# Kernel tuning notes

Hardware: AMD Instinct MI355X
Metric: run time of the kernel (lower is better)

Reference implementation:

```python
import jax, jax.numpy as jnp
import numpy as np

ALPHA, BETA, THETA = 1.0, 1.0, 10.0
WIN_SIZE = 11
SIGMA = 1.5


def _gauss_window(size, sigma, channel):
    g = np.exp(-((np.arange(size) - size // 2) ** 2) / (2.0 * sigma ** 2))
    g = g / g.sum()
    w2 = np.outer(g, g).astype(np.float32)  # [k, k]
    return jnp.asarray(np.tile(w2[None, None], (channel, 1, 1, 1)))  # [C,1,k,k]


def _dwconv_valid(x, w):
    # x: [B,C,H,W], w: [C,1,k,k]; depthwise conv, no padding (matches F.conv2d padd=0, groups=C)
    return jax.lax.conv_general_dilated(
        x, w, window_strides=(1, 1), padding='VALID',
        feature_group_count=x.shape[1],
        dimension_numbers=('NCHW', 'OIHW', 'NCHW'))


def _ssim_loss(img1, img2, window):
    # val_range heuristic: inputs in [0,1) -> L = 1
    L = 1.0
    C1 = (0.01 * L) ** 2
    C2 = (0.03 * L) ** 2
    mu1 = _dwconv_valid(img1, window)
    mu2 = _dwconv_valid(img2, window)
    mu1_sq = mu1 * mu1
    mu2_sq = mu2 * mu2
    mu1_mu2 = mu1 * mu2
    sigma1_sq = _dwconv_valid(img1 * img1, window) - mu1_sq
    sigma2_sq = _dwconv_valid(img2 * img2, window) - mu2_sq
    sigma12 = _dwconv_valid(img1 * img2, window) - mu1_mu2
    v1 = 2.0 * sigma12 + C2
    v2 = sigma1_sq + sigma2_sq + C2
    ssim_map = (2.0 * mu1_mu2 + C1) * v1 / ((mu1_sq + mu2_sq + C1) * v2)
    return 1.0 - jnp.mean(ssim_map)


_LAP2D = np.array([[1.0, 1.0, 1.0],
                   [1.0, -8.0, 1.0],
                   [1.0, 1.0, 1.0]], dtype=np.float32) / 16.0  # kornia normalized (abs-sum=16)


def _laplacian(x):
    # kornia.filters.laplacian(x, 3): reflect padding, normalized 3x3 laplacian, depthwise
    c = x.shape[1]
    k = jnp.asarray(np.tile(_LAP2D[None, None], (c, 1, 1, 1)))  # [C,1,3,3]
    xp = jnp.pad(x, ((0, 0), (0, 0), (1, 1), (1, 1)), mode='reflect')
    return _dwconv_valid(xp, k)


def setup_inputs() -> dict:
    key = jax.random.key(0)
    ks = jax.random.split(key, 5)
    shape = (32, 1, 512, 512)
    names = ['im_fus', 'im_ir', 'im_vi', 'map_ir', 'map_vi']
    return {n: jax.random.uniform(k, shape, dtype=jnp.float32) for n, k in zip(names, ks)}


def reference(im_fus, im_ir, im_vi, map_ir, map_vi):
    window = _gauss_window(WIN_SIZE, SIGMA, im_fus.shape[1])
    ms_ssim_loss = _ssim_loss(im_fus, im_ir, window) + _ssim_loss(im_fus, im_vi, window)
    l1_loss = jnp.mean(jnp.abs(jnp.maximum(map_ir, map_vi) - im_fus))
    ir_grad = jnp.abs(_laplacian(im_ir))
    vi_grad = jnp.abs(_laplacian(im_vi))
    fus_grad = jnp.abs(_laplacian(im_fus))
    grad_loss = jnp.mean(jnp.abs(jnp.maximum(ir_grad, vi_grad) - fus_grad))
    return ALPHA * ms_ssim_loss + BETA * l1_loss + THETA * grad_loss
```

## Files before the change

### kernel.cpp

```cpp
#include <hip/hip_runtime.h>
#include <cmath>


typedef float f32x2 __attribute__((ext_vector_type(2)));

struct GaussW { float w[11]; };

#define SSIM_C1 1.0e-4f
#define SSIM_C2 9.0e-4f

__global__ __launch_bounds__(256, 2)
void ssim_kernel(const float* __restrict__ fus, const float* __restrict__ irp,
                 const float* __restrict__ vip, const float* __restrict__ mir,
                 const float* __restrict__ mvi, float* __restrict__ ws,
                 GaussW gw)
{
    const int b    = blockIdx.z;
    const int rs   = blockIdx.y;
    const int r0   = rs * 42;
    const int tid  = threadIdx.x;
    const int wv   = tid >> 6;
    const int lane = tid & 63;
    const int c0   = blockIdx.x * 256 + wv * 64;
    const int out_rows = min(42, 502 - r0);
    const int in_rows  = out_rows + 10;
    const bool first = (rs == 0);
    const bool last  = (rs == 11);

    const size_t ib = (size_t)b * 512 * 512;
    const float* __restrict__ Fp = fus + ib;
    const float* __restrict__ Ip = irp + ib;
    const float* __restrict__ Vp = vip + ib;
    mir += ib;
    mvi += ib;

    __shared__ f32x2 srow_fi[4][80];
    __shared__ float srow_v [4][80];

    float w6[6];
#pragma unroll
    for (int k = 0; k < 6; ++k) w6[k] = gw.w[k];

    f32x2 acc[11][4];
#pragma unroll
    for (int s = 0; s < 11; ++s)
#pragma unroll
        for (int q = 0; q < 4; ++q) acc[s][q] = (f32x2)(0.f);

    float lssim = 0.f, l1s = 0.f, grs = 0.f;
    const int  col      = c0 + lane;
    const bool col_ok   = col <= 501;
    const bool is_left  = (lane == 10);
    const int  colH     = is_left ? (c0 - 1) : (c0 + 64 + lane);
    const bool halo_ok  = (lane < 10) ? (colH < 512) : (is_left && c0 > 0);
    const int  hidx     = 64 + lane;
    const int il       = (lane == 0) ? ((c0 == 0) ? 1 : 74) : (lane - 1);
    const bool rt_edge = (lane == 63) && (c0 + 64 >= 512);

    f32x2 csFI_1 = (f32x2)(0.f), csFI_2 = (f32x2)(0.f);
    float csV_1 = 0.f, csV_2 = 0.f;
    f32x2 cPrevFI = (f32x2)(0.f); float cPrevV = 0.f;
    float m1r = 0.f, m2r = 0.f;

    float rf, rg, rv, rf2 = 0.f, rg2 = 0.f, rv2 = 0.f;
    {
        const size_t b0 = (size_t)r0 * 512 + col;
        rf = Fp[b0]; rg = Ip[b0]; rv = Vp[b0];
        if (halo_ok) {
            const size_t bh = (size_t)r0 * 512 + colH;
            rf2 = Fp[bh]; rg2 = Ip[bh]; rv2 = Vp[bh];
        }
    }

#pragma unroll 1
    for (int rb = 0; rb < 55; rb += 11) {
#pragma unroll
        for (int p = 0; p < 11; ++p) {
            const int r = rb + p;
            if (r < in_rows) {
                const float curF = rf, curI = rg, curV = rv;
                srow_fi[wv][lane] = (f32x2){rf, rg};
                srow_v [wv][lane] = rv;
                if (halo_ok) {
                    srow_fi[wv][hidx] = (f32x2){rf2, rg2};
                    srow_v [wv][hidx] = rv2;
                }
                __builtin_amdgcn_wave_barrier();

                if (r + 1 < in_rows) {
                    const size_t base = (size_t)(r0 + r + 1) * 512 + col;
                    rf = Fp[base]; rg = Ip[base]; rv = Vp[base];
                    if (halo_ok) {
                        const size_t bh = (size_t)(r0 + r + 1) * 512 + colH;
                        rf2 = Fp[bh]; rg2 = Ip[bh]; rv2 = Vp[bh];
                    }
                }

                f32x2 hfhi  = (f32x2)(0.f);
                f32x2 hffii = (f32x2)(0.f);
                f32x2 hfifv = (f32x2)(0.f);
                f32x2 hvvv  = (f32x2)(0.f);
                f32x2 fi1 = (f32x2)(0.f); float v1 = 0.f;
#pragma unroll
                for (int k = 0; k < 11; ++k) {
                    const float t = w6[k < 6 ? k : 10 - k];
                    const f32x2 fi = srow_fi[wv][lane + k];
                    const float V  = srow_v [wv][lane + k];
                    if (k == 1) { fi1 = fi; v1 = V; }
                    const f32x2 t2 = (f32x2){t, t};
                    const f32x2 tfi = t2 * fi;
                    hfhi  = __builtin_elementwise_fma(t2,  fi, hfhi);
                    hffii = __builtin_elementwise_fma(tfi, fi, hffii);
                    hfifv.x = fmaf(tfi.x, fi.y, hfifv.x);
                    hfifv.y = fmaf(tfi.x, V,    hfifv.y);
                    const float tV = t * V;
                    hvvv.x = fmaf(t,  V, hvvv.x);
                    hvvv.y = fmaf(tV, V, hvvv.y);
                }

                const bool lap_row = (r <= 43) || last;
                f32x2 csFI_cur = (f32x2)(0.f); float csV_cur = 0.f;
                if (lap_row) {
                    const f32x2 fiL = srow_fi[wv][il];
                    const float vL  = srow_v [wv][il];
                    f32x2 fiR = fi1; float vR = v1;
                    if (rt_edge) { fiR = fiL; vR = vL; }
                    csFI_cur = fiL + fiR + (f32x2){curF, curI};
                    csV_cur  = vL  + vR  + curV;
                }
                __builtin_amdgcn_wave_barrier();

                {
                    const f32x2 w02 = (f32x2){w6[0], w6[0]};
                    acc[p][0] = w02 * hfhi;
                    acc[p][1] = w02 * hffii;
                    acc[p][2] = w02 * hfifv;
                    acc[p][3] = w02 * hvvv;
                }
#pragma unroll
                for (int k = 1; k < 11; ++k) {
                    const int s = (p - k + 11) % 11;
                    const float t = w6[k < 6 ? k : 10 - k];
                    const f32x2 t2 = (f32x2){t, t};
                    acc[s][0] = __builtin_elementwise_fma(t2, hfhi,  acc[s][0]);
                    acc[s][1] = __builtin_elementwise_fma(t2, hffii, acc[s][1]);
                    acc[s][2] = __builtin_elementwise_fma(t2, hfifv, acc[s][2]);
                    acc[s][3] = __builtin_elementwise_fma(t2, hvvv,  acc[s][3]);
                }
                if (r >= 10) {
                    const int s = (p + 1) % 11;
                    const float mu1 = acc[s][0].x, mu2 = acc[s][0].y, mu3 = acc[s][3].x;
                    const float eff = acc[s][1].x, eii = acc[s][1].y, evv = acc[s][3].y;
                    const float efi = acc[s][2].x, efv = acc[s][2].y;
                    const float mu1sq = mu1*mu1, mu2sq = mu2*mu2, mu3sq = mu3*mu3;
                    const float mu12 = mu1*mu2, mu13 = mu1*mu3;
                    const float sf  = eff - mu1sq;
                    const float si  = eii - mu2sq;
                    const float sv  = evv - mu3sq;
                    const float s12 = efi - mu12;
                    const float s13 = efv - mu13;
                    const float n1 = (2.f*mu12 + SSIM_C1) * (2.f*s12 + SSIM_C2);
                    const float d1 = (mu1sq + mu2sq + SSIM_C1) * (sf + si + SSIM_C2);
                    const float n2 = (2.f*mu13 + SSIM_C1) * (2.f*s13 + SSIM_C2);
                    const float d2 = (mu1sq + mu3sq + SSIM_C1) * (sf + sv + SSIM_C2);
                    const float q1 = __builtin_amdgcn_rcpf(d1);
                    const float q2 = __builtin_amdgcn_rcpf(d2);
                    if (col_ok) lssim += fmaf(n1, q1, n2 * q2);
                }
                if (r >= 2 && lap_row) {
                    const f32x2 sFI = csFI_2 + csFI_1 + csFI_cur;
                    const float sV  = csV_2 + csV_1 + csV_cur;
                    const f32x2 lFI = __builtin_elementwise_fma(
                                         (f32x2){-9.f,-9.f}, cPrevFI, sFI);
                    const float lV  = fmaf(-9.f, cPrevV, sV);
                    grs += fabsf(fmaxf(fabsf(lFI.y), fabsf(lV)) - fabsf(lFI.x));
                    l1s += fabsf(fmaxf(m1r, m2r) - cPrevFI.x);
                }
                if (first && r == 1) {
                    const f32x2 sFI = csFI_1 + csFI_cur + csFI_cur;
                    const float sV  = csV_1 + csV_cur + csV_cur;
                    const f32x2 lFI = __builtin_elementwise_fma(
                                         (f32x2){-9.f,-9.f}, cPrevFI, sFI);
                    const float lV  = fmaf(-9.f, cPrevV, sV);
                    grs += fabsf(fmaxf(fabsf(lFI.y), fabsf(lV)) - fabsf(lFI.x));
                    l1s += fabsf(fmaxf(m1r, m2r) - cPrevFI.x);
                }
                if (lap_row) {
                    csFI_2 = csFI_1; csFI_1 = csFI_cur;
                    csV_2  = csV_1;  csV_1  = csV_cur;
                    cPrevFI = (f32x2){curF, curI}; cPrevV = curV;
                    const int ny = min(r0 + r, 511);
                    const size_t bm = (size_t)ny * 512 + col;
                    m1r = mir[bm]; m2r = mvi[bm];
                }
            }
        }
    }

    if (last) {
        const size_t bm = (size_t)511 * 512 + col;
        const float m1e = mir[bm], m2e = mvi[bm];
        const f32x2 sFI = csFI_2 + csFI_2 + csFI_1;
        const float sV  = csV_2 + csV_2 + csV_1;
        const f32x2 lFI = __builtin_elementwise_fma((f32x2){-9.f,-9.f}, cPrevFI, sFI);
        const float lV  = fmaf(-9.f, cPrevV, sV);
        grs += fabsf(fmaxf(fabsf(lFI.y), fabsf(lV)) - fabsf(lFI.x));
        l1s += fabsf(fmaxf(m1e, m2e) - cPrevFI.x);
    }

#pragma unroll
    for (int off = 32; off > 0; off >>= 1) {
        lssim += __shfl_down(lssim, off);
        l1s   += __shfl_down(l1s, off);
        grs   += __shfl_down(grs, off);
    }
    __shared__ float red[12];
    if (lane == 0) { red[wv] = lssim; red[4 + wv] = l1s; red[8 + wv] = grs; }
    __syncthreads();
    if (tid == 0) {
        const int blk = blockIdx.x + 2 * (blockIdx.y + 12 * blockIdx.z);
        ws[blk]        = red[0] + red[1] + red[2] + red[3];
        ws[768 + blk]  = red[4] + red[5] + red[6] + red[7];
        ws[1536 + blk] = (red[8] + red[9] + red[10] + red[11]) * 0.0625f;
    }
}

__global__ void final_kernel(const float* __restrict__ ws, float* __restrict__ out)
{
    const int tid = threadIdx.x;
    float s0 = 0.f, s1 = 0.f, s2 = 0.f;
#pragma unroll
    for (int i = tid; i < 768; i += 256) {
        s0 += ws[i];
        s1 += ws[768 + i];
        s2 += ws[1536 + i];
    }
#pragma unroll
    for (int off = 32; off > 0; off >>= 1) {
        s0 += __shfl_down(s0, off);
        s1 += __shfl_down(s1, off);
        s2 += __shfl_down(s2, off);
    }
    __shared__ float red[12];
    if ((tid & 63) == 0) {
        red[tid >> 6] = s0; red[4 + (tid >> 6)] = s1; red[8 + (tid >> 6)] = s2;
    }
    __syncthreads();
    if (tid == 0) {
        const float ssim_sum = red[0] + red[1] + red[2] + red[3];
        const float l1_sum   = red[4] + red[5] + red[6] + red[7];
        const float gr_sum   = red[8] + red[9] + red[10] + red[11];
        const float ms = 2.f - ssim_sum / 8064128.f;
        const float l1 = l1_sum / 8388608.f;
        const float gr = gr_sum / 8388608.f;
        out[0] = ms + l1 + 10.f * gr;
    }
}

extern "C" void kernel_launch(void* const* d_in, const int* in_sizes, int n_in,
                              void* d_out, int out_size, void* d_ws, size_t ws_size,
                              hipStream_t stream)
{
    const float* fus = (const float*)d_in[0];
    const float* irp = (const float*)d_in[1];
    const float* vip = (const float*)d_in[2];
    const float* mir = (const float*)d_in[3];
    const float* mvi = (const float*)d_in[4];
    float* out = (float*)d_out;
    float* ws  = (float*)d_ws;

    GaussW gw;
    double g[11], s = 0.0;
    for (int i = 0; i < 11; ++i) {
        const double d = (double)i - 5.0;
        g[i] = std::exp(-(d * d) / (2.0 * 1.5 * 1.5));
        s += g[i];
    }
    for (int i = 0; i < 11; ++i) gw.w[i] = (float)(g[i] / s);

    ssim_kernel<<<dim3(2, 12, 32), 256, 0, stream>>>(fus, irp, vip, mir, mvi,
                                                     ws, gw);
    final_kernel<<<1, 256, 0, stream>>>(ws, out);
}
```

Baseline: 96.47 us.

## Process two input rows per iteration with double-row shared buffers

The row-streaming loop now handles a pair of input rows per step. Both rows are staged into separate shared-memory slots and their horizontal Gaussian sums are computed together, with the vertical accumulator ring updated once per row. The goal is to halve the number of wave barriers and loop-control overheads per row and to give the scheduler more independent global loads and FMAs to interleave. In exchange it raises register pressure, since two sets of horizontal sums and prefetched rows are live at once. It also adds complexity to the Laplacian and L1 edge handling, which is now done in pairs.

```diff
diff --git a/kernel.cpp b/kernel.cpp
--- a/kernel.cpp
+++ b/kernel.cpp
@@ -34,8 +34,8 @@
     mir += ib;
     mvi += ib;
 
-    __shared__ f32x2 srow_fi[4][80];
-    __shared__ float srow_v [4][80];
+    __shared__ f32x2 srow_fi[4][2][80];
+    __shared__ float srow_v [4][2][80];
 
     float w6[6];
 #pragma unroll
@@ -60,95 +60,123 @@
     f32x2 csFI_1 = (f32x2)(0.f), csFI_2 = (f32x2)(0.f);
     float csV_1 = 0.f, csV_2 = 0.f;
     f32x2 cPrevFI = (f32x2)(0.f); float cPrevV = 0.f;
-    float m1r = 0.f, m2r = 0.f;
-
-    float rf, rg, rv, rf2 = 0.f, rg2 = 0.f, rv2 = 0.f;
+    float mA1 = 0.f, mA2 = 0.f, mB1, mB2;
+
+    float arf, arg, arv, arf2 = 0.f, arg2 = 0.f, arv2 = 0.f;
+    float brf, brg, brv, brf2 = 0.f, brg2 = 0.f, brv2 = 0.f;
     {
         const size_t b0 = (size_t)r0 * 512 + col;
-        rf = Fp[b0]; rg = Ip[b0]; rv = Vp[b0];
+        arf = Fp[b0]; arg = Ip[b0]; arv = Vp[b0];
+        const size_t b1 = (size_t)(r0 + 1) * 512 + col;
+        brf = Fp[b1]; brg = Ip[b1]; brv = Vp[b1];
         if (halo_ok) {
-            const size_t bh = (size_t)r0 * 512 + colH;
-            rf2 = Fp[bh]; rg2 = Ip[bh]; rv2 = Vp[bh];
+            const size_t h0 = (size_t)r0 * 512 + colH;
+            arf2 = Fp[h0]; arg2 = Ip[h0]; arv2 = Vp[h0];
+            const size_t h1 = (size_t)(r0 + 1) * 512 + colH;
+            brf2 = Fp[h1]; brg2 = Ip[h1]; brv2 = Vp[h1];
         }
+        mB1 = mir[b0]; mB2 = mvi[b0];
     }
 
 #pragma unroll 1
-    for (int rb = 0; rb < 55; rb += 11) {
+    for (int rb = 0; rb < 66; rb += 22) {
 #pragma unroll
         for (int p = 0; p < 11; ++p) {
-            const int r = rb + p;
+            const int r = rb + 2 * p;
             if (r < in_rows) {
-                const float curF = rf, curI = rg, curV = rv;
-                srow_fi[wv][lane] = (f32x2){rf, rg};
-                srow_v [wv][lane] = rv;
+                srow_fi[wv][0][lane] = (f32x2){arf, arg};
+                srow_v [wv][0][lane] = arv;
+                srow_fi[wv][1][lane] = (f32x2){brf, brg};
+                srow_v [wv][1][lane] = brv;
                 if (halo_ok) {
-                    srow_fi[wv][hidx] = (f32x2){rf2, rg2};
-                    srow_v [wv][hidx] = rv2;
+                    srow_fi[wv][0][hidx] = (f32x2){arf2, arg2};
+                    srow_v [wv][0][hidx] = arv2;
+                    srow_fi[wv][1][hidx] = (f32x2){brf2, brg2};
+                    srow_v [wv][1][hidx] = brv2;
                 }
                 __builtin_amdgcn_wave_barrier();
 
-                if (r + 1 < in_rows) {
-                    const size_t base = (size_t)(r0 + r + 1) * 512 + col;
-                    rf = Fp[base]; rg = Ip[base]; rv = Vp[base];
+                if (r + 2 < in_rows) {
+                    const size_t bA = (size_t)(r0 + r + 2) * 512 + col;
+                    arf = Fp[bA]; arg = Ip[bA]; arv = Vp[bA];
+                    const size_t bB = (size_t)(r0 + r + 3) * 512 + col;
+                    brf = Fp[bB]; brg = Ip[bB]; brv = Vp[bB];
                     if (halo_ok) {
-                        const size_t bh = (size_t)(r0 + r + 1) * 512 + colH;
-                        rf2 = Fp[bh]; rg2 = Ip[bh]; rv2 = Vp[bh];
+                        const size_t hA = (size_t)(r0 + r + 2) * 512 + colH;
+                        arf2 = Fp[hA]; arg2 = Ip[hA]; arv2 = Vp[hA];
+                        const size_t hB = (size_t)(r0 + r + 3) * 512 + colH;
+                        brf2 = Fp[hB]; brg2 = Ip[hB]; brv2 = Vp[hB];
                     }
                 }
 
-                f32x2 hfhi  = (f32x2)(0.f);
-                f32x2 hffii = (f32x2)(0.f);
-                f32x2 hfifv = (f32x2)(0.f);
-                f32x2 hvvv  = (f32x2)(0.f);
-                f32x2 fi1 = (f32x2)(0.f); float v1 = 0.f;
+                f32x2 hfhiA = (f32x2)(0.f), hffiiA = (f32x2)(0.f);
+                f32x2 hfifvA = (f32x2)(0.f), hvvvA = (f32x2)(0.f);
+                f32x2 hfhiB = (f32x2)(0.f), hffiiB = (f32x2)(0.f);
+                f32x2 hfifvB = (f32x2)(0.f), hvvvB = (f32x2)(0.f);
+                f32x2 fi0A = (f32x2)(0.f), fi1A = (f32x2)(0.f);
+                f32x2 fi0B = (f32x2)(0.f), fi1B = (f32x2)(0.f);
+                float v0A = 0.f, v1A = 0.f, v0B = 0.f, v1B = 0.f;
 #pragma unroll
                 for (int k = 0; k < 11; ++k) {
                     const float t = w6[k < 6 ? k : 10 - k];
-                    const f32x2 fi = srow_fi[wv][lane + k];
-                    const float V  = srow_v [wv][lane + k];
-                    if (k == 1) { fi1 = fi; v1 = V; }
                     const f32x2 t2 = (f32x2){t, t};
-                    const f32x2 tfi = t2 * fi;
-                    hfhi  = __builtin_elementwise_fma(t2,  fi, hfhi);
-                    hffii = __builtin_elementwise_fma(tfi, fi, hffii);
-                    hfifv.x = fmaf(tfi.x, fi.y, hfifv.x);
-                    hfifv.y = fmaf(tfi.x, V,    hfifv.y);
-                    const float tV = t * V;
-                    hvvv.x = fmaf(t,  V, hvvv.x);
-                    hvvv.y = fmaf(tV, V, hvvv.y);
-                }
-
-                const bool lap_row = (r <= 43) || last;
-                f32x2 csFI_cur = (f32x2)(0.f); float csV_cur = 0.f;
-                if (lap_row) {
-                    const f32x2 fiL = srow_fi[wv][il];
-                    const float vL  = srow_v [wv][il];
-                    f32x2 fiR = fi1; float vR = v1;
-                    if (rt_edge) { fiR = fiL; vR = vL; }
-                    csFI_cur = fiL + fiR + (f32x2){curF, curI};
-                    csV_cur  = vL  + vR  + curV;
+                    const f32x2 fiA = srow_fi[wv][0][lane + k];
+                    const float VA  = srow_v [wv][0][lane + k];
+                    const f32x2 fiB = srow_fi[wv][1][lane + k];
+                    const float VB  = srow_v [wv][1][lane + k];
+                    if (k == 0) { fi0A = fiA; v0A = VA; fi0B = fiB; v0B = VB; }
+                    if (k == 1) { fi1A = fiA; v1A = VA; fi1B = fiB; v1B = VB; }
+                    const f32x2 tfiA = t2 * fiA;
+                    hfhiA  = __builtin_elementwise_fma(t2,   fiA, hfhiA);
+                    hffiiA = __builtin_elementwise_fma(tfiA, fiA, hffiiA);
+                    hfifvA.x = fmaf(tfiA.x, fiA.y, hfifvA.x);
+                    hfifvA.y = fmaf(tfiA.x, VA,    hfifvA.y);
+                    hvvvA.x = fmaf(t,      VA, hvvvA.x);
+                    hvvvA.y = fmaf(t * VA, VA, hvvvA.y);
+                    const f32x2 tfiB = t2 * fiB;
+                    hfhiB  = __builtin_elementwise_fma(t2,   fiB, hfhiB);
+                    hffiiB = __builtin_elementwise_fma(tfiB, fiB, hffiiB);
+                    hfifvB.x = fmaf(tfiB.x, fiB.y, hfifvB.x);
+                    hfifvB.y = fmaf(tfiB.x, VB,    hfifvB.y);
+                    hvvvB.x = fmaf(t,      VB, hvvvB.x);
+                    hvvvB.y = fmaf(t * VB, VB, hvvvB.y);
+                }
+
+                const bool lap = (r <= 43) || last;
+                f32x2 csA_FI = (f32x2)(0.f), csB_FI = (f32x2)(0.f);
+                float csA_V = 0.f, csB_V = 0.f;
+                if (lap) {
+                    const f32x2 fiLA = srow_fi[wv][0][il];
+                    const float vLA  = srow_v [wv][0][il];
+                    const f32x2 fiLB = srow_fi[wv][1][il];
+                    const float vLB  = srow_v [wv][1][il];
+                    f32x2 fiRA = fi1A; float vRA = v1A;
+                    f32x2 fiRB = fi1B; float vRB = v1B;
+                    if (rt_edge) { fiRA = fiLA; vRA = vLA; fiRB = fiLB; vRB = vLB; }
+                    csA_FI = fiLA + fiRA + fi0A;  csA_V = vLA + vRA + v0A;
+                    csB_FI = fiLB + fiRB + fi0B;  csB_V = vLB + vRB + v0B;
                 }
                 __builtin_amdgcn_wave_barrier();
 
                 {
                     const f32x2 w02 = (f32x2){w6[0], w6[0]};
-                    acc[p][0] = w02 * hfhi;
-                    acc[p][1] = w02 * hffii;
-                    acc[p][2] = w02 * hfifv;
-                    acc[p][3] = w02 * hvvv;
+                    acc[(2*p) % 11][0] = w02 * hfhiA;
+                    acc[(2*p) % 11][1] = w02 * hffiiA;
+                    acc[(2*p) % 11][2] = w02 * hfifvA;
+                    acc[(2*p) % 11][3] = w02 * hvvvA;
                 }
 #pragma unroll
                 for (int k = 1; k < 11; ++k) {
-                    const int s = (p - k + 11) % 11;
+                    const int s = (2*p - k + 22) % 11;
                     const float t = w6[k < 6 ? k : 10 - k];
                     const f32x2 t2 = (f32x2){t, t};
-                    acc[s][0] = __builtin_elementwise_fma(t2, hfhi,  acc[s][0]);
-                    acc[s][1] = __builtin_elementwise_fma(t2, hffii, acc[s][1]);
-                    acc[s][2] = __builtin_elementwise_fma(t2, hfifv, acc[s][2]);
-                    acc[s][3] = __builtin_elementwise_fma(t2, hvvv,  acc[s][3]);
+                    acc[s][0] = __builtin_elementwise_fma(t2, hfhiA,  acc[s][0]);
+                    acc[s][1] = __builtin_elementwise_fma(t2, hffiiA, acc[s][1]);
+                    acc[s][2] = __builtin_elementwise_fma(t2, hfifvA, acc[s][2]);
+                    acc[s][3] = __builtin_elementwise_fma(t2, hvvvA,  acc[s][3]);
                 }
                 if (r >= 10) {
-                    const int s = (p + 1) % 11;
+                    const int s = (2*p + 1) % 11;
                     const float mu1 = acc[s][0].x, mu2 = acc[s][0].y, mu3 = acc[s][3].x;
                     const float eff = acc[s][1].x, eii = acc[s][1].y, evv = acc[s][3].y;
                     const float efi = acc[s][2].x, efv = acc[s][2].y;
@@ -167,31 +195,81 @@
                     const float q2 = __builtin_amdgcn_rcpf(d2);
                     if (col_ok) lssim += fmaf(n1, q1, n2 * q2);
                 }
-                if (r >= 2 && lap_row) {
-                    const f32x2 sFI = csFI_2 + csFI_1 + csFI_cur;
-                    const float sV  = csV_2 + csV_1 + csV_cur;
-                    const f32x2 lFI = __builtin_elementwise_fma(
-                                         (f32x2){-9.f,-9.f}, cPrevFI, sFI);
-                    const float lV  = fmaf(-9.f, cPrevV, sV);
-                    grs += fabsf(fmaxf(fabsf(lFI.y), fabsf(lV)) - fabsf(lFI.x));
-                    l1s += fabsf(fmaxf(m1r, m2r) - cPrevFI.x);
-                }
-                if (first && r == 1) {
-                    const f32x2 sFI = csFI_1 + csFI_cur + csFI_cur;
-                    const float sV  = csV_1 + csV_cur + csV_cur;
-                    const f32x2 lFI = __builtin_elementwise_fma(
-                                         (f32x2){-9.f,-9.f}, cPrevFI, sFI);
-                    const float lV  = fmaf(-9.f, cPrevV, sV);
-                    grs += fabsf(fmaxf(fabsf(lFI.y), fabsf(lV)) - fabsf(lFI.x));
-                    l1s += fabsf(fmaxf(m1r, m2r) - cPrevFI.x);
-                }
-                if (lap_row) {
-                    csFI_2 = csFI_1; csFI_1 = csFI_cur;
-                    csV_2  = csV_1;  csV_1  = csV_cur;
-                    cPrevFI = (f32x2){curF, curI}; cPrevV = curV;
-                    const int ny = min(r0 + r, 511);
-                    const size_t bm = (size_t)ny * 512 + col;
-                    m1r = mir[bm]; m2r = mvi[bm];
+                {
+                    const f32x2 w02 = (f32x2){w6[0], w6[0]};
+                    acc[(2*p + 1) % 11][0] = w02 * hfhiB;
+                    acc[(2*p + 1) % 11][1] = w02 * hffiiB;
+                    acc[(2*p + 1) % 11][2] = w02 * hfifvB;
+                    acc[(2*p + 1) % 11][3] = w02 * hvvvB;
+                }
+#pragma unroll
+                for (int k = 1; k < 11; ++k) {
+                    const int s = (2*p + 1 - k + 22) % 11;
+                    const float t = w6[k < 6 ? k : 10 - k];
+                    const f32x2 t2 = (f32x2){t, t};
+                    acc[s][0] = __builtin_elementwise_fma(t2, hfhiB,  acc[s][0]);
+                    acc[s][1] = __builtin_elementwise_fma(t2, hffiiB, acc[s][1]);
+                    acc[s][2] = __builtin_elementwise_fma(t2, hfifvB, acc[s][2]);
+                    acc[s][3] = __builtin_elementwise_fma(t2, hvvvB,  acc[s][3]);
+                }
+                if (r >= 10) {
+                    const int s = (2*p + 2) % 11;
+                    const float mu1 = acc[s][0].x, mu2 = acc[s][0].y, mu3 = acc[s][3].x;
+                    const float eff = acc[s][1].x, eii = acc[s][1].y, evv = acc[s][3].y;
+                    const float efi = acc[s][2].x, efv = acc[s][2].y;
+                    const float mu1sq = mu1*mu1, mu2sq = mu2*mu2, mu3sq = mu3*mu3;
+                    const float mu12 = mu1*mu2, mu13 = mu1*mu3;
+                    const float sf  = eff - mu1sq;
+                    const float si  = eii - mu2sq;
+                    const float sv  = evv - mu3sq;
+                    const float s12 = efi - mu12;
+                    const float s13 = efv - mu13;
+                    const float n1 = (2.f*mu12 + SSIM_C1) * (2.f*s12 + SSIM_C2);
+                    const float d1 = (mu1sq + mu2sq + SSIM_C1) * (sf + si + SSIM_C2);
+                    const float n2 = (2.f*mu13 + SSIM_C1) * (2.f*s13 + SSIM_C2);
+                    const float d2 = (mu1sq + mu3sq + SSIM_C1) * (sf + sv + SSIM_C2);
+                    const float q1 = __builtin_amdgcn_rcpf(d1);
+                    const float q2 = __builtin_amdgcn_rcpf(d2);
+                    if (col_ok) lssim += fmaf(n1, q1, n2 * q2);
+                }
+
+                if (lap) {
+                    if (r >= 2) {
+                        const f32x2 sFI = csFI_2 + csFI_1 + csA_FI;
+                        const float sV  = csV_2 + csV_1 + csA_V;
+                        const f32x2 lFI = __builtin_elementwise_fma(
+                                             (f32x2){-9.f,-9.f}, cPrevFI, sFI);
+                        const float lV  = fmaf(-9.f, cPrevV, sV);
+                        grs += fabsf(fmaxf(fabsf(lFI.y), fabsf(lV)) - fabsf(lFI.x));
+                        l1s += fabsf(fmaxf(mA1, mA2) - cPrevFI.x);
+                        const f32x2 sFI2 = csFI_1 + csA_FI + csB_FI;
+                        const float sV2  = csV_1 + csA_V + csB_V;
+                        const f32x2 lFI2 = __builtin_elementwise_fma(
+                                             (f32x2){-9.f,-9.f}, fi0A, sFI2);
+                        const float lV2  = fmaf(-9.f, v0A, sV2);
+                        grs += fabsf(fmaxf(fabsf(lFI2.y), fabsf(lV2)) - fabsf(lFI2.x));
+                        l1s += fabsf(fmaxf(mB1, mB2) - fi0A.x);
+                    }
+                    if (first && r == 0) {
+                        const f32x2 sFI = csA_FI + csB_FI + csB_FI;
+                        const float sV  = csA_V + csB_V + csB_V;
+                        const f32x2 lFI = __builtin_elementwise_fma(
+                                             (f32x2){-9.f,-9.f}, fi0A, sFI);
+                        const float lV  = fmaf(-9.f, v0A, sV);
+                        grs += fabsf(fmaxf(fabsf(lFI.y), fabsf(lV)) - fabsf(lFI.x));
+                        l1s += fabsf(fmaxf(mB1, mB2) - fi0A.x);
+                    }
+                    csFI_2 = csA_FI; csFI_1 = csB_FI;
+                    csV_2  = csA_V;  csV_1  = csB_V;
+                    cPrevFI = fi0B;  cPrevV = v0B;
+                    if (r + 2 < in_rows) {
+                        const int yA = min(r0 + r + 1, 511);
+                        const int yB = min(r0 + r + 2, 511);
+                        const size_t bmA = (size_t)yA * 512 + col;
+                        const size_t bmB = (size_t)yB * 512 + col;
+                        mA1 = mir[bmA]; mA2 = mvi[bmA];
+                        mB1 = mir[bmB]; mB2 = mvi[bmB];
+                    }
                 }
             }
         }
```

New measurement: 89.97 us, median of 2. -6.7%, faster.
